# Optimization experiments

Hardware: AMD Instinct MI355X
Metric: run time of the kernel (lower is better)

The kernel has to match this reference:

```python
import jax, jax.numpy as jnp
import numpy as np

NEG_INF = float(-2**32 + 1)  # matches tf paddings = -2**32+1


def setup_inputs() -> dict:
    key = jax.random.key(0)
    k1, k2, k3 = jax.random.split(key, 3)
    B, T, U = 128, 8192, 64
    align = jax.random.normal(k1, (B, 1, T), dtype=jnp.float32)
    value = jax.random.normal(k2, (B, T, U), dtype=jnp.float32)
    key_masks = jax.random.randint(k3, (B, 1, T), 0, 2) > 0  # bool [B,1,T]
    return {"align": align, "value": value, "key_masks": key_masks}


def reference(align, value, key_masks):
    # mask-fill invalid positions with a very negative constant
    scores = jnp.where(key_masks, align, NEG_INF)           # [B,1,T]
    attn = jax.nn.softmax(scores, axis=-1)                  # [B,1,T]
    # dropout_rate=0 / inference: dropout is identity
    out = jnp.matmul(attn, value)                           # [B,1,U]
    return out
```

## Files before the change

### kernel.cpp

```cpp
#include <hip/hip_runtime.h>
#include <math.h>

#define NEG_INF_F (-4294967295.0f)

typedef float f4 __attribute__((ext_vector_type(4)));

constexpr int B_ = 128;
constexpr int T_ = 8192;
constexpr int U_ = 64;
constexpr int NCHUNK = 16;
constexpr int CHUNK  = T_ / NCHUNK;

__global__ __launch_bounds__(256) void k_fused(const float* __restrict__ align,
                                               const int* __restrict__ mask,
                                               const float* __restrict__ value,
                                               float* __restrict__ partial) {
  const int b     = blockIdx.x / NCHUNK;
  const int chunk = blockIdx.x % NCHUNK;
  const int tid   = threadIdx.x;

  const float4* a4 = (const float4*)(align + (size_t)b * T_);
  const int4*   m4 = (const int4*)(mask + (size_t)b * T_);

  float sc[32];
#pragma unroll
  for (int j = 0; j < 8; ++j) {
    const float4 av = a4[j * 256 + tid];
    const int4   mv = m4[j * 256 + tid];
    sc[j * 4 + 0] = mv.x ? av.x : NEG_INF_F;
    sc[j * 4 + 1] = mv.y ? av.y : NEG_INF_F;
    sc[j * 4 + 2] = mv.z ? av.z : NEG_INF_F;
    sc[j * 4 + 3] = mv.w ? av.w : NEG_INF_F;
  }

  float lmax = sc[0];
#pragma unroll
  for (int i = 1; i < 32; ++i) lmax = fmaxf(lmax, sc[i]);
#pragma unroll
  for (int off = 32; off > 0; off >>= 1) lmax = fmaxf(lmax, __shfl_xor(lmax, off));

  __shared__ float red[4];
  __shared__ float s_m, s_invl;
  if ((tid & 63) == 0) red[tid >> 6] = lmax;
  __syncthreads();
  if (tid == 0) s_m = fmaxf(fmaxf(red[0], red[1]), fmaxf(red[2], red[3]));
  __syncthreads();
  const float m = s_m;

  float lsum = 0.f;
#pragma unroll
  for (int i = 0; i < 32; ++i) { sc[i] = __expf(sc[i] - m); lsum += sc[i]; }
#pragma unroll
  for (int off = 32; off > 0; off >>= 1) lsum += __shfl_xor(lsum, off);
  if ((tid & 63) == 0) red[tid >> 6] = lsum;
  __syncthreads();
  if (tid == 0) s_invl = 1.0f / (red[0] + red[1] + red[2] + red[3]);
  __syncthreads();
  const float invl = s_invl;

  __shared__ float w_s[CHUNK];
  if ((tid >> 7) == (chunk & 1)) {
    const int jown = chunk >> 1;
    const int k    = tid & 127;
    ((float4*)w_s)[k] = make_float4(sc[jown * 4 + 0] * invl, sc[jown * 4 + 1] * invl,
                                    sc[jown * 4 + 2] * invl, sc[jown * 4 + 3] * invl);
  }
  __syncthreads();

  const int grp  = tid >> 4;
  const int lane = tid & 15;
  const f4* v4 = (const f4*)(value + (size_t)b * T_ * U_) +
                 (size_t)chunk * CHUNK * 16;

  f4 acc = (f4)(0.f);
#pragma unroll 4
  for (int it = 0; it < CHUNK / 16; ++it) {
    const int tl = it * 16 + grp;
    const float wt = w_s[tl];
    const f4 v = __builtin_nontemporal_load(&v4[(size_t)tl * 16 + lane]);
    acc += wt * v;
  }

  __shared__ f4 lds[16][16];
  lds[grp][lane] = acc;
  __syncthreads();
#pragma unroll
  for (int s = 8; s > 0; s >>= 1) {
    if (grp < s) {
      acc += lds[grp + s][lane];
      lds[grp][lane] = acc;
    }
    __syncthreads();
  }
  if (grp == 0) {
    f4* p = (f4*)(partial + ((size_t)b * NCHUNK + chunk) * U_);
    p[lane] = acc;
  }
}

__global__ __launch_bounds__(256) void k_final(const float* __restrict__ partial,
                                               float* __restrict__ out) {
  const int idx = blockIdx.x * blockDim.x + threadIdx.x;
  const int b = idx / U_;
  const int u = idx % U_;
  const float* p = partial + (size_t)b * NCHUNK * U_ + u;
  float s = 0.f;
#pragma unroll
  for (int c = 0; c < NCHUNK; ++c) s += p[c * U_];
  out[idx] = s;
}

extern "C" void kernel_launch(void* const* d_in, const int* in_sizes, int n_in,
                              void* d_out, int out_size, void* d_ws, size_t ws_size,
                              hipStream_t stream) {
  const float* align = (const float*)d_in[0];
  const float* value = (const float*)d_in[1];
  const int*   mask  = (const int*)d_in[2];
  float* out = (float*)d_out;

  float* partial = (float*)d_ws;

  k_fused<<<B_ * NCHUNK, 256, 0, stream>>>(align, mask, value, partial);
  k_final<<<(B_ * U_) / 256, 256, 0, stream>>>(partial, out);
}
```

Measured before the change: 57.86 us.

## Split softmax statistics into a separate pass to avoid redundant full-row reductions

```diff
diff --git a/kernel.cpp b/kernel.cpp
--- a/kernel.cpp
+++ b/kernel.cpp
@@ -8,63 +8,73 @@
 constexpr int B_ = 128;
 constexpr int T_ = 8192;
 constexpr int U_ = 64;
+constexpr int NSTAT  = 8;
 constexpr int NCHUNK = 16;
 constexpr int CHUNK  = T_ / NCHUNK;
 
-__global__ __launch_bounds__(256) void k_fused(const float* __restrict__ align,
+__global__ __launch_bounds__(256) void k_stats(const float* __restrict__ align,
                                                const int* __restrict__ mask,
-                                               const float* __restrict__ value,
-                                               float* __restrict__ partial) {
-  const int b     = blockIdx.x / NCHUNK;
-  const int chunk = blockIdx.x % NCHUNK;
-  const int tid   = threadIdx.x;
+                                               float2* __restrict__ stats) {
+  const int b   = blockIdx.x / NSTAT;
+  const int s   = blockIdx.x % NSTAT;
+  const int tid = threadIdx.x;
+  const size_t base = (size_t)b * T_ + (size_t)s * 1024;
 
-  const float4* a4 = (const float4*)(align + (size_t)b * T_);
-  const int4*   m4 = (const int4*)(mask + (size_t)b * T_);
+  const float4 av = ((const float4*)(align + base))[tid];
+  const int4   mv = ((const int4*)(mask + base))[tid];
+  float sc[4];
+  sc[0] = mv.x ? av.x : NEG_INF_F;
+  sc[1] = mv.y ? av.y : NEG_INF_F;
+  sc[2] = mv.z ? av.z : NEG_INF_F;
+  sc[3] = mv.w ? av.w : NEG_INF_F;
 
-  float sc[32];
-#pragma unroll
-  for (int j = 0; j < 8; ++j) {
-    const float4 av = a4[j * 256 + tid];
-    const int4   mv = m4[j * 256 + tid];
-    sc[j * 4 + 0] = mv.x ? av.x : NEG_INF_F;
-    sc[j * 4 + 1] = mv.y ? av.y : NEG_INF_F;
-    sc[j * 4 + 2] = mv.z ? av.z : NEG_INF_F;
-    sc[j * 4 + 3] = mv.w ? av.w : NEG_INF_F;
-  }
-
-  float lmax = sc[0];
-#pragma unroll
-  for (int i = 1; i < 32; ++i) lmax = fmaxf(lmax, sc[i]);
+  float lmax = fmaxf(fmaxf(sc[0], sc[1]), fmaxf(sc[2], sc[3]));
 #pragma unroll
   for (int off = 32; off > 0; off >>= 1) lmax = fmaxf(lmax, __shfl_xor(lmax, off));
 
   __shared__ float red[4];
-  __shared__ float s_m, s_invl;
+  __shared__ float s_m;
   if ((tid & 63) == 0) red[tid >> 6] = lmax;
   __syncthreads();
   if (tid == 0) s_m = fmaxf(fmaxf(red[0], red[1]), fmaxf(red[2], red[3]));
   __syncthreads();
   const float m = s_m;
 
-  float lsum = 0.f;
-#pragma unroll
-  for (int i = 0; i < 32; ++i) { sc[i] = __expf(sc[i] - m); lsum += sc[i]; }
+  float lsum = __expf(sc[0] - m) + __expf(sc[1] - m) +
+               __expf(sc[2] - m) + __expf(sc[3] - m);
 #pragma unroll
   for (int off = 32; off > 0; off >>= 1) lsum += __shfl_xor(lsum, off);
   if ((tid & 63) == 0) red[tid >> 6] = lsum;
   __syncthreads();
-  if (tid == 0) s_invl = 1.0f / (red[0] + red[1] + red[2] + red[3]);
-  __syncthreads();
-  const float invl = s_invl;
+  if (tid == 0) stats[blockIdx.x] = make_float2(m, red[0] + red[1] + red[2] + red[3]);
+}
 
+__global__ __launch_bounds__(256) void k_stream(const float* __restrict__ align,
+                                                const int* __restrict__ mask,
+                                                const float* __restrict__ value,
+                                                const float2* __restrict__ stats,
+                                                float* __restrict__ partial) {
+  const int b     = blockIdx.x / NCHUNK;
+  const int chunk = blockIdx.x % NCHUNK;
+  const int tid   = threadIdx.x;
+
+  const f4* st = (const f4*)(stats + (size_t)b * NSTAT);
+  const f4 s0 = st[0], s1 = st[1], s2 = st[2], s3 = st[3];
+  float m = fmaxf(fmaxf(fmaxf(s0.x, s0.z), fmaxf(s1.x, s1.z)),
+                  fmaxf(fmaxf(s2.x, s2.z), fmaxf(s3.x, s3.z)));
+  float l = s0.y * __expf(s0.x - m) + s0.w * __expf(s0.z - m) +
+            s1.y * __expf(s1.x - m) + s1.w * __expf(s1.z - m) +
+            s2.y * __expf(s2.x - m) + s2.w * __expf(s2.z - m) +
+            s3.y * __expf(s3.x - m) + s3.w * __expf(s3.z - m);
+  const float invl = 1.0f / l;
+
+  const size_t sbase = (size_t)b * T_ + (size_t)chunk * CHUNK;
+  const float2 av = ((const float2*)(align + sbase))[tid];
+  const int2   mv = ((const int2*)(mask + sbase))[tid];
   __shared__ float w_s[CHUNK];
-  if ((tid >> 7) == (chunk & 1)) {
-    const int jown = chunk >> 1;
-    const int k    = tid & 127;
-    ((float4*)w_s)[k] = make_float4(sc[jown * 4 + 0] * invl, sc[jown * 4 + 1] * invl,
-                                    sc[jown * 4 + 2] * invl, sc[jown * 4 + 3] * invl);
-  }
+  const float w0 = __expf((mv.x ? av.x : NEG_INF_F) - m) * invl;
+  const float w1 = __expf((mv.y ? av.y : NEG_INF_F) - m) * invl;
+  ((float2*)w_s)[tid] = make_float2(w0, w1);
   __syncthreads();
 
   const int grp  = tid >> 4;
@@ -118,8 +128,10 @@
   const int*   mask  = (const int*)d_in[2];
   float* out = (float*)d_out;
 
-  float* partial = (float*)d_ws;
+  float2* stats   = (float2*)d_ws;
+  float*  partial = (float*)d_ws + 2 * B_ * NSTAT;
 
-  k_fused<<<B_ * NCHUNK, 256, 0, stream>>>(align, mask, value, partial);
+  k_stats<<<B_ * NSTAT, 256, 0, stream>>>(align, mask, stats);
+  k_stream<<<B_ * NCHUNK, 256, 0, stream>>>(align, mask, value, stats, partial);
   k_final<<<(B_ * U_) / 256, 256, 0, stream>>>(partial, out);
 }
```

Result: faster. 53.54 us (-7.5%).

## Use per-wave online-softmax partials instead of redundant full-row softmax per block

Applied to the files above, without the earlier changes.

```diff
diff --git a/kernel.cpp b/kernel.cpp
--- a/kernel.cpp
+++ b/kernel.cpp
@@ -10,104 +10,98 @@
 constexpr int U_ = 64;
 constexpr int NCHUNK = 16;
 constexpr int CHUNK  = T_ / NCHUNK;
+constexpr int WROWS  = CHUNK / 4;
+constexpr int NW     = NCHUNK * 4;
 
-__global__ __launch_bounds__(256) void k_fused(const float* __restrict__ align,
-                                               const int* __restrict__ mask,
-                                               const float* __restrict__ value,
-                                               float* __restrict__ partial) {
+__global__ __launch_bounds__(256) void k_stream(const float* __restrict__ align,
+                                                const int* __restrict__ mask,
+                                                const float* __restrict__ value,
+                                                float2* __restrict__ ms,
+                                                float* __restrict__ p) {
   const int b     = blockIdx.x / NCHUNK;
   const int chunk = blockIdx.x % NCHUNK;
   const int tid   = threadIdx.x;
+  const int wid   = tid >> 6;
+  const int lane  = tid & 63;
+  const int g     = lane >> 4;
+  const int s     = lane & 15;
 
-  const float4* a4 = (const float4*)(align + (size_t)b * T_);
-  const int4*   m4 = (const int4*)(mask + (size_t)b * T_);
+  const int t0 = chunk * CHUNK + wid * WROWS;
 
-  float sc[32];
+  const size_t abase = (size_t)b * T_ + t0;
+  const float2 av = ((const float2*)(align + abase))[lane];
+  const int2   mv = ((const int2*)(mask + abase))[lane];
+  const float x0 = mv.x ? av.x : NEG_INF_F;
+  const float x1 = mv.y ? av.y : NEG_INF_F;
+
+  float m = fmaxf(x0, x1);
 #pragma unroll
-  for (int j = 0; j < 8; ++j) {
-    const float4 av = a4[j * 256 + tid];
-    const int4   mv = m4[j * 256 + tid];
-    sc[j * 4 + 0] = mv.x ? av.x : NEG_INF_F;
-    sc[j * 4 + 1] = mv.y ? av.y : NEG_INF_F;
-    sc[j * 4 + 2] = mv.z ? av.z : NEG_INF_F;
-    sc[j * 4 + 3] = mv.w ? av.w : NEG_INF_F;
-  }
+  for (int off = 32; off > 0; off >>= 1) m = fmaxf(m, __shfl_xor(m, off));
 
-  float lmax = sc[0];
+  const float e0 = __expf(x0 - m);
+  const float e1 = __expf(x1 - m);
+  float ssum = e0 + e1;
 #pragma unroll
-  for (int i = 1; i < 32; ++i) lmax = fmaxf(lmax, sc[i]);
-#pragma unroll
-  for (int off = 32; off > 0; off >>= 1) lmax = fmaxf(lmax, __shfl_xor(lmax, off));
+  for (int off = 32; off > 0; off >>= 1) ssum += __shfl_xor(ssum, off);
 
-  __shared__ float red[4];
-  __shared__ float s_m, s_invl;
-  if ((tid & 63) == 0) red[tid >> 6] = lmax;
-  __syncthreads();
-  if (tid == 0) s_m = fmaxf(fmaxf(red[0], red[1]), fmaxf(red[2], red[3]));
-  __syncthreads();
-  const float m = s_m;
-
-  float lsum = 0.f;
-#pragma unroll
-  for (int i = 0; i < 32; ++i) { sc[i] = __expf(sc[i] - m); lsum += sc[i]; }
-#pragma unroll
-  for (int off = 32; off > 0; off >>= 1) lsum += __shfl_xor(lsum, off);
-  if ((tid & 63) == 0) red[tid >> 6] = lsum;
-  __syncthreads();
-  if (tid == 0) s_invl = 1.0f / (red[0] + red[1] + red[2] + red[3]);
-  __syncthreads();
-  const float invl = s_invl;
-
-  __shared__ float w_s[CHUNK];
-  if ((tid >> 7) == (chunk & 1)) {
-    const int jown = chunk >> 1;
-    const int k    = tid & 127;
-    ((float4*)w_s)[k] = make_float4(sc[jown * 4 + 0] * invl, sc[jown * 4 + 1] * invl,
-                                    sc[jown * 4 + 2] * invl, sc[jown * 4 + 3] * invl);
-  }
+  __shared__ float w_lds[4 * WROWS];
+  ((float2*)(w_lds + wid * WROWS))[lane] = make_float2(e0, e1);
   __syncthreads();
 
-  const int grp  = tid >> 4;
-  const int lane = tid & 15;
-  const f4* v4 = (const f4*)(value + (size_t)b * T_ * U_) +
-                 (size_t)chunk * CHUNK * 16;
+  const f4* v4 = (const f4*)(value + (size_t)b * T_ * U_) + (size_t)t0 * 16;
+  const float* wl = w_lds + wid * WROWS;
 
   f4 acc = (f4)(0.f);
-#pragma unroll 4
-  for (int it = 0; it < CHUNK / 16; ++it) {
-    const int tl = it * 16 + grp;
-    const float wt = w_s[tl];
-    const f4 v = __builtin_nontemporal_load(&v4[(size_t)tl * 16 + lane]);
+#pragma unroll 8
+  for (int it = 0; it < WROWS / 4; ++it) {
+    const int r = it * 4 + g;
+    const float wt = wl[r];
+    const f4 v = __builtin_nontemporal_load(&v4[(size_t)r * 16 + s]);
     acc += wt * v;
   }
 
-  __shared__ f4 lds[16][16];
-  lds[grp][lane] = acc;
-  __syncthreads();
 #pragma unroll
-  for (int s = 8; s > 0; s >>= 1) {
-    if (grp < s) {
-      acc += lds[grp + s][lane];
-      lds[grp][lane] = acc;
-    }
-    __syncthreads();
+  for (int off = 16; off <= 32; off <<= 1) {
+    acc.x += __shfl_xor(acc.x, off);
+    acc.y += __shfl_xor(acc.y, off);
+    acc.z += __shfl_xor(acc.z, off);
+    acc.w += __shfl_xor(acc.w, off);
   }
-  if (grp == 0) {
-    f4* p = (f4*)(partial + ((size_t)b * NCHUNK + chunk) * U_);
-    p[lane] = acc;
+
+  const int wg = chunk * 4 + wid;
+  if (g == 0) {
+    f4* pp = (f4*)(p + ((size_t)b * NW + wg) * U_);
+    pp[s] = acc;
   }
+  if (lane == 0) ms[(size_t)b * NW + wg] = make_float2(m, ssum);
 }
 
-__global__ __launch_bounds__(256) void k_final(const float* __restrict__ partial,
-                                               float* __restrict__ out) {
-  const int idx = blockIdx.x * blockDim.x + threadIdx.x;
-  const int b = idx / U_;
-  const int u = idx % U_;
-  const float* p = partial + (size_t)b * NCHUNK * U_ + u;
-  float s = 0.f;
+__global__ __launch_bounds__(64) void k_final(const float2* __restrict__ ms,
+                                              const float* __restrict__ p,
+                                              float* __restrict__ out) {
+  const int b = blockIdx.x;
+  const int u = threadIdx.x;
+
+  const float2 msu = ms[(size_t)b * NW + u];
+  float m = msu.x;
 #pragma unroll
-  for (int c = 0; c < NCHUNK; ++c) s += p[c * U_];
-  out[idx] = s;
+  for (int off = 32; off > 0; off >>= 1) m = fmaxf(m, __shfl_xor(m, off));
+
+  const float e = __expf(msu.x - m);
+  float d = msu.y * e;
+#pragma unroll
+  for (int off = 32; off > 0; off >>= 1) d += __shfl_xor(d, off);
+
+  __shared__ float e_s[NW];
+  e_s[u] = e;
+  __syncthreads();
+
+  const float* pb = p + (size_t)b * NW * U_ + u;
+  float num = 0.f;
+#pragma unroll
+  for (int j = 0; j < NW; ++j) num += pb[(size_t)j * U_] * e_s[j];
+
+  out[(size_t)b * U_ + u] = num / d;
 }
 
 extern "C" void kernel_launch(void* const* d_in, const int* in_sizes, int n_in,
@@ -118,8 +112,9 @@
   const int*   mask  = (const int*)d_in[2];
   float* out = (float*)d_out;
 
-  float* partial = (float*)d_ws;
+  float2* ms = (float2*)d_ws;
+  float*  p  = (float*)d_ws + 2 * (B_ * NW);
 
-  k_fused<<<B_ * NCHUNK, 256, 0, stream>>>(align, mask, value, partial);
-  k_final<<<(B_ * U_) / 256, 256, 0, stream>>>(partial, out);
+  k_stream<<<B_ * NCHUNK, 256, 0, stream>>>(align, mask, value, ms, p);
+  k_final<<<B_, 64, 0, stream>>>(ms, p, out);
 }
```

New measurement: 50.48 us. -12.8%, faster.
